# Performance work log

Measured on AMD Instinct MI355X. Metric: run time of the kernel, lower is better.

## Reference

```python
import jax, jax.numpy as jnp
import numpy as np

B, S, T = 4, 512, 512
V, D, F, H, DK, N = 32000, 512, 2048, 8, 64, 6
PAD = 0

# sinusoidal positional encoding table, matching the torch source exactly
_pos = np.arange(max(S, T))[:, None]
_i = np.arange(D // 2)[None, :]
_ang = _pos / (10000.0 ** (2 * _i / D))
_pe = np.empty((max(S, T), D), dtype=np.float32)
_pe[:, 0::2] = np.sin(_ang)
_pe[:, 1::2] = np.cos(_ang)
PE = jnp.asarray(_pe)


def setup_inputs() -> dict:
    key = jax.random.key(0)
    ks = iter(jax.random.split(key, 64))
    s = 0.02
    w = lambda shape: jax.random.normal(next(ks), shape, jnp.float32) * s
    inp = {
        'src': jax.random.randint(next(ks), (B, S), 0, V, jnp.int32),
        'trg': jax.random.randint(next(ks), (B, T), 0, V, jnp.int32),
        'emb_src': w((V, D)).at[PAD].set(0.0),
        'emb_trg': w((V, D)).at[PAD].set(0.0),
        # encoder stacks (leading axis = layer)
        'enc_wq': w((N, D, H * DK)), 'enc_wk': w((N, D, H * DK)),
        'enc_wv': w((N, D, H * DK)), 'enc_wo': w((N, H * DK, D)),
        'enc_ln1_g': jnp.ones((N, D)), 'enc_ln1_b': jnp.zeros((N, D)),
        'enc_w1': w((N, D, F)), 'enc_b1': jnp.zeros((N, F)),
        'enc_w2': w((N, F, D)), 'enc_b2': jnp.zeros((N, D)),
        'enc_ln2_g': jnp.ones((N, D)), 'enc_ln2_b': jnp.zeros((N, D)),
        # decoder stacks
        'dec_wq': w((N, D, H * DK)), 'dec_wk': w((N, D, H * DK)),
        'dec_wv': w((N, D, H * DK)), 'dec_wo': w((N, H * DK, D)),
        'dec_ln1_g': jnp.ones((N, D)), 'dec_ln1_b': jnp.zeros((N, D)),
        'dec_cq': w((N, D, H * DK)), 'dec_ck': w((N, D, H * DK)),
        'dec_cv': w((N, D, H * DK)), 'dec_co': w((N, H * DK, D)),
        'dec_ln2_g': jnp.ones((N, D)), 'dec_ln2_b': jnp.zeros((N, D)),
        'dec_w1': w((N, D, F)), 'dec_b1': jnp.zeros((N, F)),
        'dec_w2': w((N, F, D)), 'dec_b2': jnp.zeros((N, D)),
        'dec_ln3_g': jnp.ones((N, D)), 'dec_ln3_b': jnp.zeros((N, D)),
        'proj': w((D, V)),
    }
    return inp


def _ln(x, g, b, eps=1e-5):
    m = x.mean(-1, keepdims=True)
    v = ((x - m) ** 2).mean(-1, keepdims=True)
    return (x - m) * jax.lax.rsqrt(v + eps) * g + b


def _mha(xq, xkv, wq, wk, wv, wo, mask):
    b, lq, _ = xq.shape
    lk = xkv.shape[1]
    q = (xq @ wq).reshape(b, lq, H, DK).transpose(0, 2, 1, 3)   # bhqd
    k = (xkv @ wk).reshape(b, lk, H, DK).transpose(0, 2, 1, 3)  # bhkd
    v = (xkv @ wv).reshape(b, lk, H, DK).transpose(0, 2, 1, 3)  # bhkd
    scores = jnp.einsum('bhqd,bhkd->bhqk', q, k)
    scores = jnp.where(mask, -jnp.inf, scores)
    attn = jax.nn.softmax(scores * (DK ** -0.5), axis=-1)
    out = jnp.einsum('bhqk,bhkd->bhqd', attn, v)
    out = out.transpose(0, 2, 1, 3).reshape(b, lq, H * DK)
    return out @ wo


def _ffn(x, w1, b1, w2, b2):
    return jax.nn.relu(x @ w1 + b1) @ w2 + b2


def reference(src, trg, emb_src, emb_trg,
              enc_wq, enc_wk, enc_wv, enc_wo, enc_ln1_g, enc_ln1_b,
              enc_w1, enc_b1, enc_w2, enc_b2, enc_ln2_g, enc_ln2_b,
              dec_wq, dec_wk, dec_wv, dec_wo, dec_ln1_g, dec_ln1_b,
              dec_cq, dec_ck, dec_cv, dec_co, dec_ln2_g, dec_ln2_b,
              dec_w1, dec_b1, dec_w2, dec_b2, dec_ln3_g, dec_ln3_b,
              proj):
    scale = D ** 0.5
    src_pad = (src == PAD)[:, None, None, :]                 # [B,1,1,S]
    trg_pad = (trg == PAD)[:, None, None, :]                 # [B,1,1,T]
    causal = jnp.triu(jnp.ones((T, T), bool), 1)[None, None]  # [1,1,T,T]
    trg_mask = trg_pad | causal

    # encoder (dropout = identity in eval)
    x = emb_src[src] * scale + PE[None, :S]

    def enc_step(h, p):
        wq, wk, wv, wo, g1, b1, w1, bb1, w2, bb2, g2, b2 = p
        h = _ln(h + _mha(h, h, wq, wk, wv, wo, src_pad), g1, b1)
        h = _ln(h + _ffn(h, w1, bb1, w2, bb2), g2, b2)
        return h, None

    x_enc, _ = jax.lax.scan(enc_step, x,
        (enc_wq, enc_wk, enc_wv, enc_wo, enc_ln1_g, enc_ln1_b,
         enc_w1, enc_b1, enc_w2, enc_b2, enc_ln2_g, enc_ln2_b))

    # decoder
    y = emb_trg[trg] * scale + PE[None, :T]

    def dec_step(h, p):
        (wq, wk, wv, wo, g1, b1, cq, ck, cv, co, g2, b2,
         w1, bb1, w2, bb2, g3, b3) = p
        h = _ln(h + _mha(h, h, wq, wk, wv, wo, trg_mask), g1, b1)
        h = _ln(h + _mha(h, x_enc, cq, ck, cv, co, src_pad), g2, b2)
        h = _ln(h + _ffn(h, w1, bb1, w2, bb2), g3, b3)
        return h, None

    y, _ = jax.lax.scan(dec_step, y,
        (dec_wq, dec_wk, dec_wv, dec_wo, dec_ln1_g, dec_ln1_b,
         dec_cq, dec_ck, dec_cv, dec_co, dec_ln2_g, dec_ln2_b,
         dec_w1, dec_b1, dec_w2, dec_b2, dec_ln3_g, dec_ln3_b))

    return y @ proj  # [B, T, trg_vocab]
```

## Files before the change

### kernel.cpp

```cpp
#include <hip/hip_runtime.h>
#include <math.h>

#define BBATCH 4
#define SS 512
#define DDIM 512
#define FFN 2048
#define NHEAD 8
#define DHEAD 64
#define NL 6
#define NVOC 32000
#define MTOK (BBATCH*SS)
#define PAD_ID 0
#define MSZE ((size_t)MTOK * DDIM)

typedef unsigned short u16;
typedef __attribute__((ext_vector_type(8))) short short8;
typedef __attribute__((ext_vector_type(4))) float f32x4;

__device__ __forceinline__ u16 f2bf(float f) {
    union { float f; unsigned u; } v; v.f = f;
    unsigned r = ((v.u >> 16) & 1u) + 0x7fffu;
    return (u16)((v.u + r) >> 16);
}

__device__ __forceinline__ void gload16(const u16* g, u16* l) {
    __builtin_amdgcn_global_load_lds(
        (const __attribute__((address_space(1))) void*)g,
        (__attribute__((address_space(3))) void*)l, 16, 0, 0);
}

template<int BM, int BN, int OUTBF, int RELU, int BIAS>
__device__ __forceinline__ void gemm_core(
    u16* __restrict__ AsB, u16* __restrict__ BsB,
    const u16* __restrict__ A, int lda,
    const u16* __restrict__ B, int ldb,
    void* __restrict__ Cv, int ldc,
    int row0, int col0, int K, const float* __restrict__ bias)
{
    const int tid  = threadIdx.x;
    const int lane = tid & 63;
    const int wid  = tid >> 6;
    const int wr   = wid >> 1, wc = wid & 1;
    constexpr int MF = BM / 32, NF = BN / 32, RA = BM / 64, RB = BN / 64;

    const u16* aSrc[RA]; int aOff[RA];
    #pragma unroll
    for (int r = 0; r < RA; r++) {
        int row = (tid >> 2) + r * 64;
        int slot = ((tid & 3) << 4) ^ ((row & 3) << 4);
        aSrc[r] = A + (size_t)(row0 + row) * lda + (slot >> 1);
        aOff[r] = r * 2048 + tid * 8;
    }
    const u16* bSrc[RB]; int bOff[RB];
    #pragma unroll
    for (int r = 0; r < RB; r++) {
        int row = (tid >> 2) + r * 64;
        int slot = ((tid & 3) << 4) ^ ((row & 3) << 4);
        bSrc[r] = B + (size_t)(col0 + row) * ldb + (slot >> 1);
        bOff[r] = r * 2048 + tid * 8;
    }

    f32x4 acc[MF][NF];
    const f32x4 zero = {0.f, 0.f, 0.f, 0.f};
    #pragma unroll
    for (int m = 0; m < MF; m++)
        #pragma unroll
        for (int n = 0; n < NF; n++) acc[m][n] = zero;

    const int nt = K / 32;
    #pragma unroll
    for (int r = 0; r < RA; r++) gload16(aSrc[r], AsB + aOff[r]);
    #pragma unroll
    for (int r = 0; r < RB; r++) gload16(bSrc[r], BsB + bOff[r]);
    __syncthreads();

    for (int t = 0; t < nt; t++) {
        const int cur = t & 1;
        if (t + 1 < nt) {
            u16* ad = AsB + (cur ^ 1) * (BM * 32);
            u16* bd = BsB + (cur ^ 1) * (BN * 32);
            #pragma unroll
            for (int r = 0; r < RA; r++) gload16(aSrc[r] + (t + 1) * 32, ad + aOff[r]);
            #pragma unroll
            for (int r = 0; r < RB; r++) gload16(bSrc[r] + (t + 1) * 32, bd + bOff[r]);
        }
        const u16* as = AsB + cur * (BM * 32);
        const u16* bs = BsB + cur * (BN * 32);
        short8 af[MF], bf[NF];
        #pragma unroll
        for (int m = 0; m < MF; m++) {
            int row = wr * (BM / 2) + m * 16 + (lane & 15);
            int slot = ((lane >> 4) << 4) ^ ((row & 3) << 4);
            af[m] = *(const short8*)&as[row * 32 + (slot >> 1)];
        }
        #pragma unroll
        for (int n = 0; n < NF; n++) {
            int row = wc * (BN / 2) + n * 16 + (lane & 15);
            int slot = ((lane >> 4) << 4) ^ ((row & 3) << 4);
            bf[n] = *(const short8*)&bs[row * 32 + (slot >> 1)];
        }
        __builtin_amdgcn_s_setprio(1);
        #pragma unroll
        for (int m = 0; m < MF; m++)
            #pragma unroll
            for (int n = 0; n < NF; n++)
                acc[m][n] = __builtin_amdgcn_mfma_f32_16x16x32_bf16(af[m], bf[n], acc[m][n], 0, 0, 0);
        __builtin_amdgcn_s_setprio(0);
        __syncthreads();
    }

    const int crow = row0 + wr * (BM / 2);
    const int ccol = col0 + wc * (BN / 2);
    #pragma unroll
    for (int m = 0; m < MF; m++) {
        #pragma unroll
        for (int n = 0; n < NF; n++) {
            int col = ccol + n * 16 + (lane & 15);
            float bv = BIAS ? bias[col] : 0.0f;
            #pragma unroll
            for (int i = 0; i < 4; i++) {
                int row = crow + m * 16 + ((lane >> 4) << 2) + i;
                float v = acc[m][n][i] + bv;
                if (RELU) v = fmaxf(v, 0.0f);
                if (OUTBF) ((u16*)Cv)[(size_t)row * ldc + col] = f2bf(v);
                else       ((float*)Cv)[(size_t)row * ldc + col] = v;
            }
        }
    }
}

template<int BM, int BN, int OUTBF, int RELU, int BIAS, int SWZ = 0>
__global__ __launch_bounds__(256) void mgemm(
    const u16* __restrict__ A, int lda, size_t aSb, size_t aSh,
    const u16* __restrict__ B, int ldb, size_t bSb, size_t bSh,
    void* __restrict__ Cv, int ldc, size_t cSb, size_t cSh,
    int K, const float* __restrict__ bias)
{
    __shared__ __align__(16) u16 As[2 * BM * 32];
    __shared__ __align__(16) u16 Bs[2 * BN * 32];
    int bx = blockIdx.x, by = blockIdx.y;
    if (SWZ) {
        int nwg = gridDim.x * gridDim.y;
        int lin = by * gridDim.x + bx;
        int cpx = nwg >> 3;
        int s = (lin & 7) * cpx + (lin >> 3);
        bx = s % gridDim.x; by = s / gridDim.x;
    }
    const int zb = blockIdx.z >> 3, zh = blockIdx.z & 7;
    const u16* Ab = A + (size_t)zb * aSb + (size_t)zh * aSh;
    const u16* Bb = B + (size_t)zb * bSb + (size_t)zh * bSh;
    void* Cb = OUTBF ? (void*)((u16*)Cv + (size_t)zb * cSb + (size_t)zh * cSh)
                     : (void*)((float*)Cv + (size_t)zb * cSb + (size_t)zh * cSh);
    gemm_core<BM, BN, OUTBF, RELU, BIAS>(As, Bs, Ab, lda, Bb, ldb, Cb, ldc,
                                          by * BM, bx * BN, K, bias);
}

template<int BM, int BN>
__global__ __launch_bounds__(256) void mgemm_dual(
    const u16* __restrict__ A1, int lda1, const u16* __restrict__ B1, int ldb1,
    u16* __restrict__ C1, int ldc1, int nx1, int nblk1,
    const u16* __restrict__ A2, int lda2, const u16* __restrict__ B2, int ldb2,
    u16* __restrict__ C2, int ldc2, int nx2,
    int K)
{
    __shared__ __align__(16) u16 As[2 * BM * 32];
    __shared__ __align__(16) u16 Bs[2 * BN * 32];
    int id = blockIdx.x;
    if (id < nblk1) {
        gemm_core<BM, BN, 1, 0, 0>(As, Bs, A1, lda1, B1, ldb1, C1, ldc1,
                                    (id / nx1) * BM, (id % nx1) * BN, K, nullptr);
    } else {
        id -= nblk1;
        gemm_core<BM, BN, 1, 0, 0>(As, Bs, A2, lda2, B2, ldb2, C2, ldc2,
                                    (id / nx2) * BM, (id % nx2) * BN, K, nullptr);
    }
}

template<int CAUSAL>
__global__ __launch_bounds__(512) void flash_attn(
    const u16* __restrict__ Qp, int ldq,
    const u16* __restrict__ Kp, int ldk,
    const u16* __restrict__ Vtp,
    u16* __restrict__ O,
    const int* __restrict__ ids)
{
    __shared__ __align__(16) u16 Kl[2][64 * 64];
    __shared__ __align__(16) u16 Vl[2][64 * 64];
    __shared__ __align__(16) u16 Pl[8][16 * 64];
    __shared__ float msk[SS];

    const int tid = threadIdx.x, lane = tid & 63, wid = tid >> 6;
    const int bh = blockIdx.y, b = bh >> 3, h = bh & 7;
    const int q0 = blockIdx.x * 128;

    for (int i = tid; i < SS; i += 512)
        msk[i] = (ids[b * SS + i] == PAD_ID) ? -1e30f : 0.0f;

    const int qloc = wid * 16 + (lane & 15);
    const u16* Qb = Qp + (size_t)(b * SS + q0 + qloc) * ldq + h * 64 + ((lane >> 4) * 8);
    short8 qf[2];
    qf[0] = *(const short8*)(Qb);
    qf[1] = *(const short8*)(Qb + 32);

    const u16* Kb = Kp + (size_t)b * SS * ldk + h * 64;
    const u16* Vb = Vtp + (size_t)(h * 64) * MTOK + b * SS;

    auto stage = [&](int buf, int kt) {
        int row = tid >> 3;
        int sl  = tid & 7;
        int ls = sl ^ (row & 7);
        gload16(Kb + (size_t)(kt * 64 + row) * ldk + ls * 8, &Kl[buf][row * 64 + sl * 8]);
        gload16(Vb + (size_t)row * MTOK + kt * 64 + ls * 8, &Vl[buf][row * 64 + sl * 8]);
    };

    const int nt = CAUSAL ? (2 * blockIdx.x + 2) : (SS / 64);
    stage(0, 0);
    __syncthreads();

    float m_i[4], l_i[4];
    f32x4 o_acc[4];
    const f32x4 zero = {0.f, 0.f, 0.f, 0.f};
    #pragma unroll
    for (int i = 0; i < 4; i++) { m_i[i] = -1e30f; l_i[i] = 0.0f; }
    #pragma unroll
    for (int n = 0; n < 4; n++) o_acc[n] = zero;

    for (int kt = 0; kt < nt; kt++) {
        int cur = kt & 1;
        if (kt + 1 < nt) stage(cur ^ 1, kt + 1);

        f32x4 s_acc[4];
        #pragma unroll
        for (int n = 0; n < 4; n++) s_acc[n] = zero;
        __builtin_amdgcn_s_setprio(1);
        #pragma unroll
        for (int kk = 0; kk < 2; kk++) {
            #pragma unroll
            for (int n = 0; n < 4; n++) {
                int row = n * 16 + (lane & 15);
                int ls = (kk * 4 + (lane >> 4)) ^ (row & 7);
                short8 kf = *(const short8*)&Kl[cur][row * 64 + ls * 8];
                s_acc[n] = __builtin_amdgcn_mfma_f32_16x16x32_bf16(qf[kk], kf, s_acc[n], 0, 0, 0);
            }
        }
        __builtin_amdgcn_s_setprio(0);

        float sv[4][4];
        #pragma unroll
        for (int n = 0; n < 4; n++) {
            int kg = kt * 64 + n * 16 + (lane & 15);
            float mk = msk[kg];
            #pragma unroll
            for (int i = 0; i < 4; i++) {
                float s = s_acc[n][i] * 0.125f + mk;
                if (CAUSAL) {
                    int qg = q0 + wid * 16 + ((lane >> 4) << 2) + i;
                    if (kg > qg) s = -1e30f;
                }
                sv[n][i] = s;
            }
        }
        float pm[4], mn[4], rs[4], ps[4];
        #pragma unroll
        for (int i = 0; i < 4; i++)
            pm[i] = fmaxf(fmaxf(sv[0][i], sv[1][i]), fmaxf(sv[2][i], sv[3][i]));
        #pragma unroll
        for (int i = 0; i < 4; i++) {
            #pragma unroll
            for (int msh = 1; msh <= 8; msh <<= 1)
                pm[i] = fmaxf(pm[i], __shfl_xor(pm[i], msh));
            mn[i] = fmaxf(m_i[i], pm[i]);
            rs[i] = __expf(m_i[i] - mn[i]);
            m_i[i] = mn[i];
        }
        float p[4][4];
        #pragma unroll
        for (int n = 0; n < 4; n++)
            #pragma unroll
            for (int i = 0; i < 4; i++)
                p[n][i] = (sv[n][i] < -1e29f) ? 0.0f : __expf(sv[n][i] - mn[i]);
        #pragma unroll
        for (int i = 0; i < 4; i++) {
            ps[i] = p[0][i] + p[1][i] + p[2][i] + p[3][i];
            #pragma unroll
            for (int msh = 1; msh <= 8; msh <<= 1)
                ps[i] += __shfl_xor(ps[i], msh);
            l_i[i] = l_i[i] * rs[i] + ps[i];
        }
        #pragma unroll
        for (int n = 0; n < 4; n++)
            #pragma unroll
            for (int i = 0; i < 4; i++)
                o_acc[n][i] *= rs[i];

        #pragma unroll
        for (int n = 0; n < 4; n++) {
            int k = n * 16 + (lane & 15);
            #pragma unroll
            for (int i = 0; i < 4; i++) {
                int q = ((lane >> 4) << 2) + i;
                Pl[wid][q * 64 + (((k >> 3) ^ (q & 7)) << 3) + (k & 7)] = f2bf(p[n][i]);
            }
        }
        asm volatile("s_waitcnt lgkmcnt(0)" ::: "memory");
        __builtin_amdgcn_sched_barrier(0);

        __builtin_amdgcn_s_setprio(1);
        #pragma unroll
        for (int kk = 0; kk < 2; kk++) {
            int qrow = lane & 15;
            int lsp = (kk * 4 + (lane >> 4)) ^ (qrow & 7);
            short8 pa = *(const short8*)&Pl[wid][qrow * 64 + lsp * 8];
            #pragma unroll
            for (int nf = 0; nf < 4; nf++) {
                int row = nf * 16 + (lane & 15);
                int vs = (kk * 4 + (lane >> 4)) ^ (row & 7);
                short8 vf = *(const short8*)&Vl[cur][row * 64 + vs * 8];
                o_acc[nf] = __builtin_amdgcn_mfma_f32_16x16x32_bf16(pa, vf, o_acc[nf], 0, 0, 0);
            }
        }
        __builtin_amdgcn_s_setprio(0);
        __syncthreads();
    }

    #pragma unroll
    for (int nf = 0; nf < 4; nf++) {
        int d = h * 64 + nf * 16 + (lane & 15);
        #pragma unroll
        for (int i = 0; i < 4; i++) {
            int qg = b * SS + q0 + wid * 16 + ((lane >> 4) << 2) + i;
            O[(size_t)qg * DDIM + d] = f2bf(o_acc[nf][i] / l_i[i]);
        }
    }
}

__device__ __forceinline__ void transp_core(const float* __restrict__ src, u16* __restrict__ dst,
                                            int N, int K, int n0, int k0)
{
    __shared__ u16 t[64][65];
    const int tid = threadIdx.x;
    #pragma unroll
    for (int i = 0; i < 16; i++) {
        int idx = tid + i * 256;
        int kr = idx >> 6, nc = idx & 63;
        t[kr][nc] = f2bf(src[(size_t)(k0 + kr) * N + n0 + nc]);
    }
    __syncthreads();
    #pragma unroll
    for (int i = 0; i < 16; i++) {
        int idx = tid + i * 256;
        int nr = idx >> 6, kc = idx & 63;
        dst[(size_t)(n0 + nr) * K + k0 + kc] = t[kc][nr];
    }
}

__global__ __launch_bounds__(256) void transp(const float* __restrict__ src, u16* __restrict__ dst,
                                              int N, int K, size_t sStride, size_t dStride)
{
    transp_core(src + (size_t)blockIdx.z * sStride, dst + (size_t)blockIdx.z * dStride,
                N, K, blockIdx.x * 64, blockIdx.y * 64);
}

#define OFF_QK 0u
#define OFF_WV 524288u
#define OFF_WO 786432u
#define OFF_CQ 1048576u
#define OFF_CK 1310720u
#define OFF_CV 1572864u
#define OFF_CO 1835008u
#define OFF_W1 2097152u
#define OFF_W2 3145728u
#define WBLK   4194304u
#define M2CNT  262144u
#define MF1CNT 1048576u

__global__ __launch_bounds__(256) void transpW(
    const float* p0, const float* p1, const float* p2, const float* p3,
    const float* p4, const float* p5, const float* p6, const float* p7,
    const float* p8, const float* p9, const float* p10, const float* p11,
    u16* __restrict__ wreg)
{
    int z = blockIdx.z;
    int w = z % 12, l = z / 12;
    const float* ptrs[12] = {p0,p1,p2,p3,p4,p5,p6,p7,p8,p9,p10,p11};
    const float* src = ptrs[w] + (size_t)l * M2CNT;
    u16* dst = wreg + (w < 4 ? (size_t)l * WBLK + (size_t)w * M2CNT
                             : (size_t)(NL + l) * WBLK + (size_t)(w - 4) * M2CNT);
    transp_core(src, dst, 512, 512, blockIdx.x * 64, blockIdx.y * 64);
}

__global__ __launch_bounds__(256) void transpF1(const float* __restrict__ e,
                                                const float* __restrict__ d, u16* __restrict__ wreg)
{
    int z = blockIdx.z; int l = z % NL, w = z / NL;
    const float* src = (w ? d : e) + (size_t)l * MF1CNT;
    u16* dst = wreg + (size_t)(w * NL + l) * WBLK + OFF_W1;
    transp_core(src, dst, 2048, 512, blockIdx.x * 64, blockIdx.y * 64);
}

__global__ __launch_bounds__(256) void transpF2(const float* __restrict__ e,
                                                const float* __restrict__ d, u16* __restrict__ wreg)
{
    int z = blockIdx.z; int l = z % NL, w = z / NL;
    const float* src = (w ? d : e) + (size_t)l * MF1CNT;
    u16* dst = wreg + (size_t)(w * NL + l) * WBLK + OFF_W2;
    transp_core(src, dst, 512, 2048, blockIdx.x * 64, blockIdx.y * 64);
}

__global__ void pe_kernel(float* __restrict__ PEt)
{
    int pos = blockIdx.x, d = threadIdx.x;
    int i = d >> 1;
    double freq = exp(-(2.0 * (double)i / (double)DDIM) * log(10000.0));
    double ang = (double)pos * freq;
    PEt[pos * DDIM + d] = (float)((d & 1) ? cos(ang) : sin(ang));
}

__global__ void embed_kernel(const int* __restrict__ src, const int* __restrict__ trg,
                             const float* __restrict__ es, const float* __restrict__ et,
                             const float* __restrict__ PEt,
                             float* __restrict__ X, u16* __restrict__ Xb,
                             float* __restrict__ Y, u16* __restrict__ Ybf)
{
    int gtok = blockIdx.x;
    int d = threadIdx.x;
    bool dec = gtok >= MTOK;
    int tok = dec ? gtok - MTOK : gtok;
    int pos = tok & (SS - 1);
    int id = (dec ? trg : src)[tok];
    const float* emb = dec ? et : es;
    float val = emb[(size_t)id * DDIM + d] * 22.62741699796952f + PEt[pos * DDIM + d];
    (dec ? Y : X)[(size_t)tok * DDIM + d] = val;
    (dec ? Ybf : Xb)[(size_t)tok * DDIM + d] = f2bf(val);
}

__global__ __launch_bounds__(256) void add_ln_kernel(float* __restrict__ x,
    const float* __restrict__ addv, const float* __restrict__ g,
    const float* __restrict__ bta, u16* __restrict__ xb)
{
    int row = blockIdx.x;
    int tid = threadIdx.x;
    size_t base = (size_t)row * DDIM;
    __shared__ float sbuf[4];

    float v0 = x[base + tid]       + addv[base + tid];
    float v1 = x[base + tid + 256] + addv[base + tid + 256];

    float s = v0 + v1;
    #pragma unroll
    for (int o = 32; o > 0; o >>= 1) s += __shfl_down(s, o);
    if ((tid & 63) == 0) sbuf[tid >> 6] = s;
    __syncthreads();
    float mean = (sbuf[0] + sbuf[1] + sbuf[2] + sbuf[3]) * (1.0f / DDIM);
    __syncthreads();

    float d0 = v0 - mean, d1 = v1 - mean;
    float ss = d0 * d0 + d1 * d1;
    #pragma unroll
    for (int o = 32; o > 0; o >>= 1) ss += __shfl_down(ss, o);
    if ((tid & 63) == 0) sbuf[tid >> 6] = ss;
    __syncthreads();
    float var = (sbuf[0] + sbuf[1] + sbuf[2] + sbuf[3]) * (1.0f / DDIM);
    float inv = rsqrtf(var + 1e-5f);

    float o0 = d0 * inv * g[tid]       + bta[tid];
    float o1 = d1 * inv * g[tid + 256] + bta[tid + 256];
    x[base + tid] = o0;
    x[base + tid + 256] = o1;
    xb[base + tid] = f2bf(o0);
    xb[base + tid + 256] = f2bf(o1);
}

__global__ __launch_bounds__(256) void add_ln_red(float* __restrict__ x,
    const float* __restrict__ part, const float* __restrict__ bias,
    const float* __restrict__ g, const float* __restrict__ bta, u16* __restrict__ xb)
{
    int row = blockIdx.x;
    int tid = threadIdx.x;
    size_t base = (size_t)row * DDIM;
    __shared__ float sbuf[4];

    float v0 = x[base + tid]       + bias[tid];
    float v1 = x[base + tid + 256] + bias[tid + 256];
    #pragma unroll
    for (int s4 = 0; s4 < 4; s4++) {
        v0 += part[s4 * MSZE + base + tid];
        v1 += part[s4 * MSZE + base + tid + 256];
    }

    float s = v0 + v1;
    #pragma unroll
    for (int o = 32; o > 0; o >>= 1) s += __shfl_down(s, o);
    if ((tid & 63) == 0) sbuf[tid >> 6] = s;
    __syncthreads();
    float mean = (sbuf[0] + sbuf[1] + sbuf[2] + sbuf[3]) * (1.0f / DDIM);
    __syncthreads();

    float d0 = v0 - mean, d1 = v1 - mean;
    float ss = d0 * d0 + d1 * d1;
    #pragma unroll
    for (int o = 32; o > 0; o >>= 1) ss += __shfl_down(ss, o);
    if ((tid & 63) == 0) sbuf[tid >> 6] = ss;
    __syncthreads();
    float var = (sbuf[0] + sbuf[1] + sbuf[2] + sbuf[3]) * (1.0f / DDIM);
    float inv = rsqrtf(var + 1e-5f);

    float o0 = d0 * inv * g[tid]       + bta[tid];
    float o1 = d1 * inv * g[tid + 256] + bta[tid + 256];
    x[base + tid] = o0;
    x[base + tid + 256] = o1;
    xb[base + tid] = f2bf(o0);
    xb[base + tid + 256] = f2bf(o1);
}

extern "C" void kernel_launch(void* const* d_in, const int* in_sizes, int n_in,
                              void* d_out, int out_size, void* d_ws, size_t ws_size,
                              hipStream_t stream)
{
    (void)in_sizes; (void)n_in; (void)out_size;

    const int*   src      = (const int*)  d_in[0];
    const int*   trg      = (const int*)  d_in[1];
    const float* emb_src  = (const float*)d_in[2];
    const float* emb_trg  = (const float*)d_in[3];
    const float* enc_wq   = (const float*)d_in[4];
    const float* enc_wk   = (const float*)d_in[5];
    const float* enc_wv   = (const float*)d_in[6];
    const float* enc_wo   = (const float*)d_in[7];
    const float* enc_ln1g = (const float*)d_in[8];
    const float* enc_ln1b = (const float*)d_in[9];
    const float* enc_w1   = (const float*)d_in[10];
    const float* enc_b1   = (const float*)d_in[11];
    const float* enc_w2   = (const float*)d_in[12];
    const float* enc_b2   = (const float*)d_in[13];
    const float* enc_ln2g = (const float*)d_in[14];
    const float* enc_ln2b = (const float*)d_in[15];
    const float* dec_wq   = (const float*)d_in[16];
    const float* dec_wk   = (const float*)d_in[17];
    const float* dec_wv   = (const float*)d_in[18];
    const float* dec_wo   = (const float*)d_in[19];
    const float* dec_ln1g = (const float*)d_in[20];
    const float* dec_ln1b = (const float*)d_in[21];
    const float* dec_cq   = (const float*)d_in[22];
    const float* dec_ck   = (const float*)d_in[23];
    const float* dec_cv   = (const float*)d_in[24];
    const float* dec_co   = (const float*)d_in[25];
    const float* dec_ln2g = (const float*)d_in[26];
    const float* dec_ln2b = (const float*)d_in[27];
    const float* dec_w1   = (const float*)d_in[28];
    const float* dec_b1   = (const float*)d_in[29];
    const float* dec_w2   = (const float*)d_in[30];
    const float* dec_b2   = (const float*)d_in[31];
    const float* dec_ln3g = (const float*)d_in[32];
    const float* dec_ln3b = (const float*)d_in[33];
    const float* proj     = (const float*)d_in[34];

    float* OUT = (float*)d_out;
    char* base = (char*)d_ws;

    size_t off = 0;
    auto carve = [&](size_t bytes) { char* p = base + off; off += (bytes + 255) & ~(size_t)255; return p; };

    float* X      = (float*)carve(MSZE * 4);
    float* Yb     = (float*)carve(MSZE * 4);
    float* T1     = (float*)carve(MSZE * 4);
    u16*   Xb     = (u16*)  carve(MSZE * 2);
    u16*   Ybf    = (u16*)  carve(MSZE * 2);
    u16*   QKb    = (u16*)  carve((size_t)MTOK * 1024 * 2);
    u16*   Vt     = (u16*)  carve((size_t)512 * MTOK * 2);
    u16*   CTX    = (u16*)  carve(MSZE * 2);
    u16*   HFF    = (u16*)  carve((size_t)MTOK * FFN * 2);
    u16*   Kcr    = (u16*)  carve((size_t)NL * MTOK * 512 * 2);
    u16*   Vtc    = (u16*)  carve((size_t)NL * 512 * MTOK * 2);
    u16*   projT  = (u16*)  carve((size_t)NVOC * 512 * 2);
    float* PEt    = (float*)carve((size_t)SS * DDIM * 4);
    float* Tp4    = (float*)carve((size_t)4 * MSZE * 4);

    const size_t WFULL_B = (size_t)12 * WBLK * 2;
    bool full = (ws_size >= off + WFULL_B);
    u16* Wreg = (u16*)carve(full ? WFULL_B : (size_t)WBLK * 2);

    auto T = [&](const float* s, u16* d, int Kd, int Nd, size_t ss, size_t ds, int L) {
        transp<<<dim3(Nd / 64, Kd / 64, L), 256, 0, stream>>>(s, d, Nd, Kd, ss, ds);
    };

    pe_kernel<<<SS, DDIM, 0, stream>>>(PEt);
    T(proj, projT, 512, NVOC, 0, 0, 1);
    if (full) {
        transpW<<<dim3(8, 8, 12 * NL), 256, 0, stream>>>(
            enc_wq, enc_wk, enc_wv, enc_wo,
            dec_wq, dec_wk, dec_wv, dec_wo,
            dec_cq, dec_ck, dec_cv, dec_co, Wreg);
        transpF1<<<dim3(32, 8, 2 * NL), 256, 0, stream>>>(enc_w1, dec_w1, Wreg);
        transpF2<<<dim3(8, 32, 2 * NL), 256, 0, stream>>>(enc_w2, dec_w2, Wreg);
    }
    embed_kernel<<<2 * MTOK, DDIM, 0, stream>>>(src, trg, emb_src, emb_trg, PEt, X, Xb, Yb, Ybf);

    auto self_attn = [&](const u16* xsrc, const u16* wb, const int* mask_ids, int causal) {
        mgemm_dual<128, 128><<<dim3(192), 256, 0, stream>>>(
            xsrc, 512, wb + OFF_QK, 512, QKb, 1024, 8, 128,
            wb + OFF_WV, 512, xsrc, 512, Vt, MTOK, 16,
            512);
        if (causal)
            flash_attn<1><<<dim3(4, 32), 512, 0, stream>>>(QKb, 1024, QKb + 512, 1024, Vt, CTX, mask_ids);
        else
            flash_attn<0><<<dim3(4, 32), 512, 0, stream>>>(QKb, 1024, QKb + 512, 1024, Vt, CTX, mask_ids);
        mgemm<64, 64, 0, 0, 0><<<dim3(8, 32, 1), 256, 0, stream>>>(
            CTX, 512, 0, 0, wb + OFF_WO, 512, 0, 0, T1, 512, 0, 0, 512, nullptr);
    };

    auto ffn = [&](const u16* xsrc, const u16* wb, const float* b1) {
        mgemm<128, 128, 1, 1, 1><<<dim3(16, 16, 1), 256, 0, stream>>>(
            xsrc, 512, 0, 0, wb + OFF_W1, 512, 0, 0, HFF, FFN, 0, 0, 512, b1);
        mgemm<128, 128, 0, 0, 0><<<dim3(4, 16, 4), 256, 0, stream>>>(
            HFF, 2048, 0, 512, wb + OFF_W2, 2048, 0, 512,
            Tp4, 512, 0, MSZE, 512, nullptr);
    };

    const size_t M2 = M2CNT, MF1 = MF1CNT;

    for (int l = 0; l < NL; l++) {
        u16* wb;
        if (full) wb = Wreg + (size_t)l * WBLK;
        else {
            wb = Wreg;
            T(enc_wq + l * M2,  wb + OFF_QK,          512, 512,  0, 0, 1);
            T(enc_wk + l * M2,  wb + OFF_QK + M2,     512, 512,  0, 0, 1);
            T(enc_wv + l * M2,  wb + OFF_WV,          512, 512,  0, 0, 1);
            T(enc_wo + l * M2,  wb + OFF_WO,          512, 512,  0, 0, 1);
            T(enc_w1 + l * MF1, wb + OFF_W1,          512, 2048, 0, 0, 1);
            T(enc_w2 + l * MF1, wb + OFF_W2,          2048, 512, 0, 0, 1);
        }
        self_attn(Xb, wb, src, 0);
        add_ln_kernel<<<MTOK, 256, 0, stream>>>(X, T1, enc_ln1g + l * DDIM, enc_ln1b + l * DDIM, Xb);
        ffn(Xb, wb, enc_b1 + l * FFN);
        add_ln_red<<<MTOK, 256, 0, stream>>>(X, Tp4, enc_b2 + l * DDIM,
                                             enc_ln2g + l * DDIM, enc_ln2b + l * DDIM, Xb);
    }

    if (full) {
        u16* Wd = Wreg + (size_t)NL * WBLK;
        mgemm<128, 128, 1, 0, 0><<<dim3(4, 16, NL), 256, 0, stream>>>(
            Xb, 512, 0, 0, Wd + OFF_CK, 512, 0, WBLK, Kcr, 512, 0, (size_t)MTOK * 512, 512, nullptr);
        mgemm<128, 128, 1, 0, 0><<<dim3(16, 4, NL), 256, 0, stream>>>(
            Wd + OFF_CV, 512, 0, WBLK, Xb, 512, 0, 0, Vtc, MTOK, 0, (size_t)512 * MTOK, 512, nullptr);
    }

    for (int l = 0; l < NL; l++) {
        u16* wb;
        if (full) wb = Wreg + (size_t)(NL + l) * WBLK;
        else {
            wb = Wreg;
            T(dec_wq + l * M2,  wb + OFF_QK,          512, 512,  0, 0, 1);
            T(dec_wk + l * M2,  wb + OFF_QK + M2,     512, 512,  0, 0, 1);
            T(dec_wv + l * M2,  wb + OFF_WV,          512, 512,  0, 0, 1);
            T(dec_wo + l * M2,  wb + OFF_WO,          512, 512,  0, 0, 1);
            T(dec_cq + l * M2,  wb + OFF_CQ,          512, 512,  0, 0, 1);
            T(dec_ck + l * M2,  wb + OFF_CK,          512, 512,  0, 0, 1);
            T(dec_cv + l * M2,  wb + OFF_CV,          512, 512,  0, 0, 1);
            T(dec_co + l * M2,  wb + OFF_CO,          512, 512,  0, 0, 1);
            T(dec_w1 + l * MF1, wb + OFF_W1,          512, 2048, 0, 0, 1);
            T(dec_w2 + l * MF1, wb + OFF_W2,          2048, 512, 0, 0, 1);
            mgemm<128, 128, 1, 0, 0><<<dim3(4, 16, 1), 256, 0, stream>>>(
                Xb, 512, 0, 0, wb + OFF_CK, 512, 0, 0, Kcr + (size_t)l * MTOK * 512, 512, 0, 0, 512, nullptr);
            mgemm<128, 128, 1, 0, 0><<<dim3(16, 4, 1), 256, 0, stream>>>(
                wb + OFF_CV, 512, 0, 0, Xb, 512, 0, 0, Vtc + (size_t)l * 512 * MTOK, MTOK, 0, 0, 512, nullptr);
        }
        self_attn(Ybf, wb, trg, 1);
        add_ln_kernel<<<MTOK, 256, 0, stream>>>(Yb, T1, dec_ln1g + l * DDIM, dec_ln1b + l * DDIM, Ybf);
        mgemm<64, 64, 1, 0, 0><<<dim3(8, 32, 1), 256, 0, stream>>>(
            Ybf, 512, 0, 0, wb + OFF_CQ, 512, 0, 0, QKb, 1024, 0, 0, 512, nullptr);
        flash_attn<0><<<dim3(4, 32), 512, 0, stream>>>(
            QKb, 1024, Kcr + (size_t)l * MTOK * 512, 512, Vtc + (size_t)l * 512 * MTOK, CTX, src);
        mgemm<64, 64, 0, 0, 0><<<dim3(8, 32, 1), 256, 0, stream>>>(
            CTX, 512, 0, 0, wb + OFF_CO, 512, 0, 0, T1, 512, 0, 0, 512, nullptr);
        add_ln_kernel<<<MTOK, 256, 0, stream>>>(Yb, T1, dec_ln2g + l * DDIM, dec_ln2b + l * DDIM, Ybf);
        ffn(Ybf, wb, dec_b1 + l * FFN);
        add_ln_red<<<MTOK, 256, 0, stream>>>(Yb, Tp4, dec_b2 + l * DDIM,
                                             dec_ln3g + l * DDIM, dec_ln3b + l * DDIM, Ybf);
    }

    mgemm<128, 128, 0, 0, 0, 1><<<dim3(NVOC / 128, 16, 1), 256, 0, stream>>>(
        Ybf, 512, 0, 0, projT, 512, 0, 0, OUT, NVOC, 0, 0, 512, nullptr);
}
```

Before: 1.573 ms.

## Deepen GEMM and attention LDS pipelines with explicit vmcnt waits

The GEMM core moves from a double-buffered to a four-buffer LDS ring with three tiles in flight. A fine-grained s_waitcnt vmcnt plus a raw s_barrier replaces the per-iteration __syncthreads. The flash attention kernel gets a three-stage K/V ring with the same scheme. The goal is to hide global-load latency behind MFMA work, at the cost of more LDS per block (lower occupancy) and fragile hand-counted wait values.

After: 1.547 ms. Within noise of the previous version (-1.6%).

```diff
diff --git a/kernel.cpp b/kernel.cpp
--- a/kernel.cpp
+++ b/kernel.cpp
@@ -29,6 +29,20 @@
         (__attribute__((address_space(3))) void*)l, 16, 0, 0);
 }
 
+template<int N> __device__ __forceinline__ void waitv() {
+    if constexpr (N == 0)      asm volatile("s_waitcnt vmcnt(0)" ::: "memory");
+    else if constexpr (N == 2) asm volatile("s_waitcnt vmcnt(2)" ::: "memory");
+    else if constexpr (N == 3) asm volatile("s_waitcnt vmcnt(3)" ::: "memory");
+    else if constexpr (N == 4) asm volatile("s_waitcnt vmcnt(4)" ::: "memory");
+    else if constexpr (N == 6) asm volatile("s_waitcnt vmcnt(6)" ::: "memory");
+    else if constexpr (N == 8) asm volatile("s_waitcnt vmcnt(8)" ::: "memory");
+    __builtin_amdgcn_sched_barrier(0);
+}
+__device__ __forceinline__ void rawbar() {
+    __builtin_amdgcn_s_barrier();
+    __builtin_amdgcn_sched_barrier(0);
+}
+
 template<int BM, int BN, int OUTBF, int RELU, int BIAS>
 __device__ __forceinline__ void gemm_core(
     u16* __restrict__ AsB, u16* __restrict__ BsB,
@@ -42,6 +56,7 @@
     const int wid  = tid >> 6;
     const int wr   = wid >> 1, wc = wid & 1;
     constexpr int MF = BM / 32, NF = BN / 32, RA = BM / 64, RB = BN / 64;
+    constexpr int LPT = RA + RB;
 
     const u16* aSrc[RA]; int aOff[RA];
     #pragma unroll
@@ -67,25 +82,17 @@
         #pragma unroll
         for (int n = 0; n < NF; n++) acc[m][n] = zero;
 
-    const int nt = K / 32;
-    #pragma unroll
-    for (int r = 0; r < RA; r++) gload16(aSrc[r], AsB + aOff[r]);
-    #pragma unroll
-    for (int r = 0; r < RB; r++) gload16(bSrc[r], BsB + bOff[r]);
-    __syncthreads();
-
-    for (int t = 0; t < nt; t++) {
-        const int cur = t & 1;
-        if (t + 1 < nt) {
-            u16* ad = AsB + (cur ^ 1) * (BM * 32);
-            u16* bd = BsB + (cur ^ 1) * (BN * 32);
-            #pragma unroll
-            for (int r = 0; r < RA; r++) gload16(aSrc[r] + (t + 1) * 32, ad + aOff[r]);
-            #pragma unroll
-            for (int r = 0; r < RB; r++) gload16(bSrc[r] + (t + 1) * 32, bd + bOff[r]);
-        }
-        const u16* as = AsB + cur * (BM * 32);
-        const u16* bs = BsB + cur * (BN * 32);
+    auto issue = [&](int t) {
+        u16* ad = AsB + (t & 3) * (BM * 32);
+        u16* bd = BsB + (t & 3) * (BN * 32);
+        #pragma unroll
+        for (int r = 0; r < RA; r++) gload16(aSrc[r] + t * 32, ad + aOff[r]);
+        #pragma unroll
+        for (int r = 0; r < RB; r++) gload16(bSrc[r] + t * 32, bd + bOff[r]);
+    };
+    auto comp = [&](int t) {
+        const u16* as = AsB + (t & 3) * (BM * 32);
+        const u16* bs = BsB + (t & 3) * (BN * 32);
         short8 af[MF], bf[NF];
         #pragma unroll
         for (int m = 0; m < MF; m++) {
@@ -106,8 +113,19 @@
             for (int n = 0; n < NF; n++)
                 acc[m][n] = __builtin_amdgcn_mfma_f32_16x16x32_bf16(af[m], bf[n], acc[m][n], 0, 0, 0);
         __builtin_amdgcn_s_setprio(0);
-        __syncthreads();
-    }
+    };
+
+    const int nt = K / 32;
+    issue(0); issue(1); issue(2);
+    int t = 0;
+    for (; t < nt - 2; ++t) {
+        waitv<2 * LPT>();
+        rawbar();
+        if (t + 3 < nt) issue(t + 3);
+        comp(t);
+    }
+    waitv<LPT>(); rawbar(); comp(nt - 2);
+    waitv<0>();   rawbar(); comp(nt - 1);
 
     const int crow = row0 + wr * (BM / 2);
     const int ccol = col0 + wc * (BN / 2);
@@ -136,8 +154,8 @@
     void* __restrict__ Cv, int ldc, size_t cSb, size_t cSh,
     int K, const float* __restrict__ bias)
 {
-    __shared__ __align__(16) u16 As[2 * BM * 32];
-    __shared__ __align__(16) u16 Bs[2 * BN * 32];
+    __shared__ __align__(16) u16 As[4 * BM * 32];
+    __shared__ __align__(16) u16 Bs[4 * BN * 32];
     int bx = blockIdx.x, by = blockIdx.y;
     if (SWZ) {
         int nwg = gridDim.x * gridDim.y;
@@ -163,8 +181,8 @@
     u16* __restrict__ C2, int ldc2, int nx2,
     int K)
 {
-    __shared__ __align__(16) u16 As[2 * BM * 32];
-    __shared__ __align__(16) u16 Bs[2 * BN * 32];
+    __shared__ __align__(16) u16 As[4 * BM * 32];
+    __shared__ __align__(16) u16 Bs[4 * BN * 32];
     int id = blockIdx.x;
     if (id < nblk1) {
         gemm_core<BM, BN, 1, 0, 0>(As, Bs, A1, lda1, B1, ldb1, C1, ldc1,
@@ -184,8 +202,8 @@
     u16* __restrict__ O,
     const int* __restrict__ ids)
 {
-    __shared__ __align__(16) u16 Kl[2][64 * 64];
-    __shared__ __align__(16) u16 Vl[2][64 * 64];
+    __shared__ __align__(16) u16 Kl[3][64 * 64];
+    __shared__ __align__(16) u16 Vl[3][64 * 64];
     __shared__ __align__(16) u16 Pl[8][16 * 64];
     __shared__ float msk[SS];
 
@@ -214,8 +232,6 @@
     };
 
     const int nt = CAUSAL ? (2 * blockIdx.x + 2) : (SS / 64);
-    stage(0, 0);
-    __syncthreads();
 
     float m_i[4], l_i[4];
     f32x4 o_acc[4];
@@ -225,10 +241,8 @@
     #pragma unroll
     for (int n = 0; n < 4; n++) o_acc[n] = zero;
 
-    for (int kt = 0; kt < nt; kt++) {
-        int cur = kt & 1;
-        if (kt + 1 < nt) stage(cur ^ 1, kt + 1);
-
+    auto comp = [&](int kt) {
+        const int cur = kt % 3;
         f32x4 s_acc[4];
         #pragma unroll
         for (int n = 0; n < 4; n++) s_acc[n] = zero;
@@ -320,8 +334,18 @@
             }
         }
         __builtin_amdgcn_s_setprio(0);
-        __syncthreads();
-    }
+    };
+
+    stage(0, 0);
+    stage(1, 1);
+    int t = 0;
+    for (; t < nt - 1; ++t) {
+        waitv<2>();
+        rawbar();
+        if (t + 2 < nt) stage((t + 2) % 3, t + 2);
+        comp(t);
+    }
+    waitv<0>(); rawbar(); comp(nt - 1);
 
     #pragma unroll
     for (int nf = 0; nf < 4; nf++) {
```
